# Kernel optimization log

Measured on AMD Instinct MI355X. Metric: run time of the kernel, lower is better.

## Reference

```python
import jax, jax.numpy as jnp
import numpy as np

B, C, N, H = 4, 256, 1024, 8
D = C            # per-head q/k dim (out_channels defaults to in_channels)
DV = C           # per-head value/output dim (y_out_channels defaults to out_channels)


def setup_inputs() -> dict:
    key = jax.random.key(0)
    ks = jax.random.split(key, 10)
    s = 0.02
    return {
        "x": jax.random.normal(ks[0], (B, C, N), jnp.float32),
        "y": jax.random.normal(ks[1], (B, C, N), jnp.float32),
        "Wq": jax.random.normal(ks[2], (H * D, C), jnp.float32) * s,
        "bq": jnp.zeros((H * D,), jnp.float32),
        "Wk": jax.random.normal(ks[3], (H * D, C), jnp.float32) * s,
        "bk": jnp.zeros((H * D,), jnp.float32),
        "Wv": jax.random.normal(ks[4], (H * DV, C), jnp.float32) * s,
        "bv": jnp.zeros((H * DV,), jnp.float32),
        "Wp": jax.random.normal(ks[5], (DV, C), jnp.float32) * s,  # projection, bias=False
        "gamma": jax.random.uniform(ks[6], (H, 1, 1, 1), jnp.float32) + 0.001,
    }


def _pconv(t, W, b):
    # 1x1 conv1d: (O,C) x (B,C,N) -> (B,O,N)
    out = jnp.einsum('oc,bcn->bon', W, t)
    return out if b is None else out + b[None, :, None]


def reference(x, y, Wq, bq, Wk, bk, Wv, bv, Wp, gamma):
    b_, _, n_ = x.shape
    h = gamma.shape[0]
    # Q/K/V projections, split channels into h heads (head-major chunks of D)
    q = _pconv(x, Wq, bq).reshape(b_, h, -1, n_)   # [B,H,D,N]
    k = _pconv(x, Wk, bk).reshape(b_, h, -1, n_)   # [B,H,D,N]
    v = _pconv(y, Wv, bv).reshape(b_, h, -1, n_)   # [B,H,DV,N]
    # energy[i,j] = sum_d q[d,i]*k[d,j]; softmax over keys j (no sqrt(d) scaling)
    attn = jax.nn.softmax(jnp.einsum('bhdn,bhdm->bhnm', q, k), axis=-1)
    out = jnp.einsum('bhdm,bhnm->bhdn', v, attn)   # [B,H,DV,N]
    # residual branch: y projected to DV channels (1x1 conv, no bias)
    yp = jnp.einsum('oc,bcn->bon', Wp, y)          # [B,DV,N]
    g = gamma.reshape(1, h, 1, 1)
    out = (g * out + yp[:, None, :, :]) / (1.0 + g)
    # concat heads along channel dim (head-major), matching split_cat(out,1,0,2)
    return out.reshape(b_, -1, n_)                 # [B,H*DV,N]
```

## Files before the change

kernel.cpp:

```cpp
#include <hip/hip_runtime.h>

#define Bb 4
#define Cc 256
#define Nn 1024
#define Hh 8
#define Oo 2048

typedef __attribute__((ext_vector_type(8))) short bf16x8;
typedef __attribute__((ext_vector_type(4))) float f32x4;

__device__ __forceinline__ short f2bf(float f) {
  unsigned u = __builtin_bit_cast(unsigned, f);
  unsigned r = u + 0x7FFFu + ((u >> 16) & 1u);
  return (short)(r >> 16);
}
__device__ __forceinline__ f32x4 mfma16(bf16x8 a, bf16x8 b, f32x4 c) {
  return __builtin_amdgcn_mfma_f32_16x16x32_bf16(a, b, c, 0, 0, 0);
}
__device__ __forceinline__ void gl_lds16(const void* g, void* l) {
  __builtin_amdgcn_global_load_lds(
      (const __attribute__((address_space(1))) void*)g,
      (__attribute__((address_space(3))) void*)l, 16, 0, 0);
}

__device__ __forceinline__ void stage_row512(const char* gbase, char* lds,
                                             int wave, int lane) {
#pragma unroll
  for (int i = 0; i < 8; i++) {
    int off = (wave * 8 + i) * 1024;
    int L = off + lane * 16;
    int r = L >> 9;
    int c = ((L >> 4) & 31) ^ (r & 7);
    gl_lds16(gbase + r * 512 + c * 16, lds + off);
  }
}
__device__ __forceinline__ void stage_row512_8(const char* gbase, char* lds,
                                               int wave, int lane) {
#pragma unroll
  for (int i = 0; i < 4; i++) {
    int off = (wave * 4 + i) * 1024;
    int L = off + lane * 16;
    int r = L >> 9;
    int c = ((L >> 4) & 31) ^ (r & 7);
    gl_lds16(gbase + r * 512 + c * 16, lds + off);
  }
}
__device__ __forceinline__ void stage_v8(const char* Vg, char* lds, int k0,
                                         int wave, int lane) {
#pragma unroll
  for (int i = 0; i < 4; i++) {
    int off = (wave * 4 + i) * 1024;
    int L = off + lane * 16;
    int r = L >> 7;
    int c = ((L >> 4) & 7) ^ (r & 7);
    gl_lds16(Vg + (size_t)r * 2048 + k0 * 2 + c * 16, lds + off);
  }
}

__global__ __launch_bounds__(256) void k_transpose(
    const float* __restrict__ x, const float* __restrict__ y,
    short* __restrict__ xT, short* __restrict__ yT,
    const float* __restrict__ Wq, const float* __restrict__ Wk,
    const float* __restrict__ Wv, const float* __restrict__ Wp,
    short* __restrict__ dWq, short* __restrict__ dWk, short* __restrict__ dWv,
    short* __restrict__ dWp) {
  {
    const int NW = Oo * Cc;
    int lin = blockIdx.x + 16 * (blockIdx.y + 4 * blockIdx.z);
    for (int i = (lin * 256 + threadIdx.x) * 4; i < 3 * NW + Cc * Cc;
         i += 512 * 256 * 4) {
      const float* src;
      short* dst;
      int off;
      if (i < NW) {
        src = Wq; dst = dWq; off = i;
      } else if (i < 2 * NW) {
        src = Wk; dst = dWk; off = i - NW;
      } else if (i < 3 * NW) {
        src = Wv; dst = dWv; off = i - 2 * NW;
      } else {
        src = Wp; dst = dWp; off = i - 3 * NW;
      }
      float4 v = *(const float4*)(src + off);
      short4 o;
      o.x = f2bf(v.x);
      o.y = f2bf(v.y);
      o.z = f2bf(v.z);
      o.w = f2bf(v.w);
      *(short4*)(dst + off) = o;
    }
  }
  int bz = blockIdx.z;
  int b = bz >> 1;
  const float* src = (bz & 1) ? y : x;
  short* dst = (bz & 1) ? yT : xT;
  src += (size_t)b * Cc * Nn;
  dst += (size_t)b * Nn * Cc;
  __shared__ short tile[64][68];
  int n0 = blockIdx.x * 64, c0 = blockIdx.y * 64;
  int t = threadIdx.x;
#pragma unroll
  for (int i = 0; i < 4; i++) {
    int idx = t + i * 256;
    int cc = idx >> 4, ng = idx & 15;
    float4 v = *(const float4*)(src + (size_t)(c0 + cc) * Nn + n0 + ng * 4);
    short4 o;
    o.x = f2bf(v.x);
    o.y = f2bf(v.y);
    o.z = f2bf(v.z);
    o.w = f2bf(v.w);
    *(short4*)&tile[cc][ng * 4] = o;
  }
  __syncthreads();
#pragma unroll
  for (int i = 0; i < 4; i++) {
    int idx = t + i * 256;
    int nn = idx >> 4, c4 = idx & 15;
    short4 o;
    o.x = tile[c4 * 4 + 0][nn];
    o.y = tile[c4 * 4 + 1][nn];
    o.z = tile[c4 * 4 + 2][nn];
    o.w = tile[c4 * 4 + 3][nn];
    *(short4*)(dst + (size_t)(n0 + nn) * Cc + c0 + c4 * 4) = o;
  }
}

__global__ __launch_bounds__(256, 4) void k_proj(
    const short* __restrict__ xT, const short* __restrict__ yT,
    const short* __restrict__ Wqb, const float* __restrict__ bq,
    const short* __restrict__ Wkb, const float* __restrict__ bk,
    const short* __restrict__ Wvb, const float* __restrict__ bv,
    const short* __restrict__ Wpb, short* __restrict__ Qt,
    short* __restrict__ Kt, short* __restrict__ Vv, float* __restrict__ yp) {
  int b = blockIdx.z, n0 = blockIdx.x * 64;
  int yb = blockIdx.y;
  int path = yb >> 5;
  int o0 = (yb & 31) * 64;
  const short* W = path == 0 ? Wqb : path == 1 ? Wkb : path == 2 ? Wvb : Wpb;
  bool dataStaged = path >= 2;
  int wave = threadIdx.x >> 6, lane = threadIdx.x & 63;
  int quad = lane >> 4, l16 = lane & 15;
  int sw = l16 & 7;
  __shared__ short Ws[64 * 256];

  const char* stage_src =
      dataStaged ? (const char*)(yT + (size_t)b * Nn * Cc + (size_t)n0 * Cc)
                 : (const char*)(W + (size_t)o0 * Cc);
  stage_row512(stage_src, (char*)Ws, wave, lane);

  const short* aptr =
      dataStaged
          ? W + (size_t)(o0 + wave * 16 + l16) * Cc + quad * 8
          : xT + (size_t)b * Nn * Cc + (size_t)(n0 + wave * 16 + l16) * Cc +
                quad * 8;
  bf16x8 areg[8];
#pragma unroll
  for (int ks = 0; ks < 8; ks++) areg[ks] = *(const bf16x8*)(aptr + ks * 32);

  f32x4 acc[4];
#pragma unroll
  for (int j = 0; j < 4; j++) acc[j] = f32x4{0.f, 0.f, 0.f, 0.f};
  __syncthreads();
#pragma unroll
  for (int ks = 0; ks < 8; ks++) {
#pragma unroll
    for (int cj = 0; cj < 4; cj++) {
      int off = (cj * 16 + l16) * 512 + (((ks * 4 + quad) ^ sw) << 4);
      bf16x8 wf = *(const bf16x8*)((const char*)Ws + off);
      if (dataStaged)
        acc[cj] = mfma16(areg[ks], wf, acc[cj]);
      else
        acc[cj] = mfma16(wf, areg[ks], acc[cj]);
    }
  }
  if (path < 2) {
    short* Od = path == 0 ? Qt : Kt;
    const float* bias = path == 0 ? bq : bk;
#pragma unroll
    for (int cj = 0; cj < 4; cj++) {
      int obase = o0 + cj * 16 + quad * 4;
      int h = obase >> 8, d = obase & 255;
      int n = n0 + wave * 16 + l16;
      float4 vb = *(const float4*)(bias + obase);
      size_t idx = (((size_t)(b * Hh + h) * Nn) + n) * 256 + d;
      short4 o;
      o.x = f2bf(acc[cj][0] + vb.x);
      o.y = f2bf(acc[cj][1] + vb.y);
      o.z = f2bf(acc[cj][2] + vb.z);
      o.w = f2bf(acc[cj][3] + vb.w);
      *(short4*)(Od + idx) = o;
    }
  } else {
#pragma unroll
    for (int cj = 0; cj < 4; cj++) {
      int n = n0 + cj * 16 + l16;
#pragma unroll
      for (int r = 0; r < 4; r++) {
        int o = o0 + wave * 16 + quad * 4 + r;
        if (path == 3) {
          yp[((size_t)b * Cc + o) * Nn + n] = acc[cj][r];
        } else {
          float v = acc[cj][r] + bv[o];
          Vv[((size_t)b * Oo + o) * Nn + n] = f2bf(v);
        }
      }
    }
  }
}

__global__ __launch_bounds__(512, 4) void k_attn(
    const short* __restrict__ Qt, const short* __restrict__ Kt,
    const short* __restrict__ Vv, const float* __restrict__ yp,
    const float* __restrict__ gamma, float* __restrict__ out) {
  int id = blockIdx.x;
  int bh = (id & 7) * 4 + (id >> 7);
  int q0 = ((id >> 3) & 15) * 64;
  int b = bh >> 3, h = bh & 7;
  int wave = threadIdx.x >> 6, lane = threadIdx.x & 63;
  int wq = wave >> 1, wk = wave & 1;
  int quad = lane >> 4, l16 = lane & 15;
  int sw = l16 & 7;
  const short* Qb = Qt + (size_t)bh * Nn * 256;
  const char* Kg = (const char*)(Kt + (size_t)bh * Nn * 256);
  const char* Vg = (const char*)(Vv + (size_t)bh * 256 * Nn);

  __shared__ short Klds[64 * 256];
  __shared__ short Vlds[256 * 64];
  __shared__ short plds[4][16][64];
  __shared__ float llds[2][64];

  bf16x8 qreg[8];
  {
    const short* qp = Qb + (size_t)(q0 + wq * 16 + l16) * 256 + quad * 8;
#pragma unroll
    for (int ks = 0; ks < 8; ks++) qreg[ks] = *(const bf16x8*)(qp + ks * 32);
  }
  f32x4 oacc[8];
#pragma unroll
  for (int j = 0; j < 8; j++) oacc[j] = f32x4{0.f, 0.f, 0.f, 0.f};
  float l_i[4] = {0.f, 0.f, 0.f, 0.f};

  stage_row512_8(Kg, (char*)Klds, wave, lane);
  stage_v8(Vg, (char*)Vlds, 0, wave, lane);

  for (int kt = 0; kt < 16; kt++) {
    int k0 = kt * 64;
    __syncthreads();
    f32x4 sc[2];
#pragma unroll
    for (int j = 0; j < 2; j++) sc[j] = f32x4{0.f, 0.f, 0.f, 0.f};
#pragma unroll
    for (int ks = 0; ks < 8; ks++) {
      bf16x8 kb0 = *(const bf16x8*)((const char*)Klds +
                                    (wk * 32 + l16) * 512 +
                                    (((ks * 4 + quad) ^ sw) << 4));
      bf16x8 kb1 = *(const bf16x8*)((const char*)Klds +
                                    (wk * 32 + 16 + l16) * 512 +
                                    (((ks * 4 + quad) ^ sw) << 4));
      sc[0] = mfma16(qreg[ks], kb0, sc[0]);
      sc[1] = mfma16(qreg[ks], kb1, sc[1]);
    }
#pragma unroll
    for (int cj = 0; cj < 2; cj++) {
#pragma unroll
      for (int r = 0; r < 4; r++) {
        float p = __expf(sc[cj][r]);
        l_i[r] += p;
        int row = quad * 4 + r;
        int keyhi = wk * 4 + cj * 2 + (l16 >> 3);
        plds[wq][row][((keyhi ^ (row & 7)) << 3) | sw] = f2bf(p);
      }
    }
    __syncthreads();
    if (kt < 15)
      stage_row512_8(Kg + (size_t)(k0 + 64) * 512, (char*)Klds, wave, lane);
#pragma unroll
    for (int c = 0; c < 2; c++) {
      bf16x8 ap[4];
#pragma unroll
      for (int qb = 0; qb < 4; qb++)
        ap[qb] = *(const bf16x8*)&plds[qb][l16][((c * 4 + quad) ^ sw) << 3];
#pragma unroll
      for (int dj = 0; dj < 2; dj++) {
        const char* vrow =
            (const char*)Vlds + (wave * 32 + dj * 16 + l16) * 128;
        bf16x8 v = *(const bf16x8*)(vrow + (((c * 4 + quad) ^ sw) << 4));
#pragma unroll
        for (int qb = 0; qb < 4; qb++)
          oacc[qb * 2 + dj] = mfma16(ap[qb], v, oacc[qb * 2 + dj]);
      }
    }
    __syncthreads();
    if (kt < 15) stage_v8(Vg, (char*)Vlds, k0 + 64, wave, lane);
  }
#pragma unroll
  for (int r = 0; r < 4; r++) {
    float v = l_i[r];
    v += __shfl_xor(v, 1);
    v += __shfl_xor(v, 2);
    v += __shfl_xor(v, 4);
    v += __shfl_xor(v, 8);
    l_i[r] = v;
  }
  if (l16 == 0) {
    f32x4 lv;
#pragma unroll
    for (int r = 0; r < 4; r++) lv[r] = l_i[r];
    *(f32x4*)&llds[wk][wq * 16 + quad * 4] = lv;
  }
  __syncthreads();
  float gf = gamma[h];
  float sg = gf / (1.f + gf), sy = 1.f / (1.f + gf);
#pragma unroll
  for (int qb = 0; qb < 4; qb++) {
    f32x4 lva = *(const f32x4*)&llds[0][qb * 16 + quad * 4];
    f32x4 lvb = *(const f32x4*)&llds[1][qb * 16 + quad * 4];
    int qq = q0 + qb * 16 + quad * 4;
#pragma unroll
    for (int dj = 0; dj < 2; dj++) {
      int dv = wave * 32 + dj * 16 + l16;
      const float* ypp = yp + ((size_t)b * 256 + dv) * Nn + qq;
      float* op = out + ((size_t)b * Oo + h * 256 + dv) * Nn + qq;
      float4 yv = *(const float4*)ypp;
      f32x4 oa = oacc[qb * 2 + dj];
      float4 ov;
      ov.x = sg * (oa[0] / (lva[0] + lvb[0])) + sy * yv.x;
      ov.y = sg * (oa[1] / (lva[1] + lvb[1])) + sy * yv.y;
      ov.z = sg * (oa[2] / (lva[2] + lvb[2])) + sy * yv.z;
      ov.w = sg * (oa[3] / (lva[3] + lvb[3])) + sy * yv.w;
      *(float4*)op = ov;
    }
  }
}

extern "C" void kernel_launch(void* const* d_in, const int* in_sizes, int n_in,
                              void* d_out, int out_size, void* d_ws,
                              size_t ws_size, hipStream_t stream) {
  const float* x = (const float*)d_in[0];
  const float* y = (const float*)d_in[1];
  const float* Wq = (const float*)d_in[2];
  const float* bq = (const float*)d_in[3];
  const float* Wk = (const float*)d_in[4];
  const float* bk = (const float*)d_in[5];
  const float* Wv = (const float*)d_in[6];
  const float* bv = (const float*)d_in[7];
  const float* Wp = (const float*)d_in[8];
  const float* gamma = (const float*)d_in[9];
  float* out = (float*)d_out;

  char* w = (char*)d_ws;
  short* Qt = (short*)(w + 0);
  short* Kt = (short*)(w + 16777216);
  short* Vv = (short*)(w + 33554432);
  short* xT = (short*)(w + 50331648);
  short* yT = (short*)(w + 52428800);
  float* yp = (float*)(w + 54525952);
  short* Wqb = (short*)(w + 58720256);
  short* Wkb = (short*)(w + 59768832);
  short* Wvb = (short*)(w + 60817408);
  short* Wpb = (short*)(w + 61865984);

  k_transpose<<<dim3(Nn / 64, Cc / 64, 2 * Bb), dim3(256), 0, stream>>>(
      x, y, xT, yT, Wq, Wk, Wv, Wp, Wqb, Wkb, Wvb, Wpb);
  k_proj<<<dim3(Nn / 64, 100, Bb), dim3(256), 0, stream>>>(
      xT, yT, Wqb, bq, Wkb, bk, Wvb, bv, Wpb, Qt, Kt, Vv, yp);
  k_attn<<<dim3(512), dim3(512), 0, stream>>>(Qt, Kt, Vv, yp, gamma, out);
}
```

Before: 192.2 us.

## Load V fragments straight from global into registers and restructure P/V work split

The attention kernel no longer stages V tiles through LDS. Each wave now loads its V fragments directly from global memory into registers, software-pipelined two deep across the head-dim blocks. The QK^T MFMA operands are swapped so P lands transposed and can be packed as bf16 pairs into a smaller LDS buffer. Each wave now owns a 16-query by 128-dim output tile instead of 64 by 32, which drops one barrier per key tile and the V LDS traffic. In exchange it adds uncoalesced, strided global reads of V that now sit on the critical path.

```diff
diff --git a/kernel.cpp b/kernel.cpp
--- a/kernel.cpp
+++ b/kernel.cpp
@@ -13,6 +13,10 @@
   unsigned u = __builtin_bit_cast(unsigned, f);
   unsigned r = u + 0x7FFFu + ((u >> 16) & 1u);
   return (short)(r >> 16);
+}
+__device__ __forceinline__ unsigned pk2(float a, float b) {
+  return ((unsigned)(unsigned short)f2bf(b) << 16) |
+         (unsigned)(unsigned short)f2bf(a);
 }
 __device__ __forceinline__ f32x4 mfma16(bf16x8 a, bf16x8 b, f32x4 c) {
   return __builtin_amdgcn_mfma_f32_16x16x32_bf16(a, b, c, 0, 0, 0);
@@ -43,17 +47,6 @@
     int r = L >> 9;
     int c = ((L >> 4) & 31) ^ (r & 7);
     gl_lds16(gbase + r * 512 + c * 16, lds + off);
-  }
-}
-__device__ __forceinline__ void stage_v8(const char* Vg, char* lds, int k0,
-                                         int wave, int lane) {
-#pragma unroll
-  for (int i = 0; i < 4; i++) {
-    int off = (wave * 4 + i) * 1024;
-    int L = off + lane * 16;
-    int r = L >> 7;
-    int c = ((L >> 4) & 7) ^ (r & 7);
-    gl_lds16(Vg + (size_t)r * 2048 + k0 * 2 + c * 16, lds + off);
   }
 }
 
@@ -225,8 +218,7 @@
   const char* Vg = (const char*)(Vv + (size_t)bh * 256 * Nn);
 
   __shared__ short Klds[64 * 256];
-  __shared__ short Vlds[256 * 64];
-  __shared__ short plds[4][16][64];
+  __shared__ unsigned plds32[4][16][36];
   __shared__ float llds[2][64];
 
   bf16x8 qreg[8];
@@ -238,17 +230,24 @@
   f32x4 oacc[8];
 #pragma unroll
   for (int j = 0; j < 8; j++) oacc[j] = f32x4{0.f, 0.f, 0.f, 0.f};
-  float l_i[4] = {0.f, 0.f, 0.f, 0.f};
+  float l_i = 0.f;
+
+  const char* vb0 = Vg + (size_t)(wk * 128 + l16) * 2048 + quad * 16;
 
   stage_row512_8(Kg, (char*)Klds, wave, lane);
-  stage_v8(Vg, (char*)Vlds, 0, wave, lane);
 
   for (int kt = 0; kt < 16; kt++) {
     int k0 = kt * 64;
     __syncthreads();
+    const char* vb = vb0 + (size_t)k0 * 2;
+    bf16x8 vf[2][2];
+    vf[0][0] = *(const bf16x8*)(vb);
+    vf[0][1] = *(const bf16x8*)(vb + 64);
+    vf[1][0] = *(const bf16x8*)(vb + 32768);
+    vf[1][1] = *(const bf16x8*)(vb + 32768 + 64);
     f32x4 sc[2];
-#pragma unroll
-    for (int j = 0; j < 2; j++) sc[j] = f32x4{0.f, 0.f, 0.f, 0.f};
+    sc[0] = f32x4{0.f, 0.f, 0.f, 0.f};
+    sc[1] = f32x4{0.f, 0.f, 0.f, 0.f};
 #pragma unroll
     for (int ks = 0; ks < 8; ks++) {
       bf16x8 kb0 = *(const bf16x8*)((const char*)Klds +
@@ -257,79 +256,65 @@
       bf16x8 kb1 = *(const bf16x8*)((const char*)Klds +
                                     (wk * 32 + 16 + l16) * 512 +
                                     (((ks * 4 + quad) ^ sw) << 4));
-      sc[0] = mfma16(qreg[ks], kb0, sc[0]);
-      sc[1] = mfma16(qreg[ks], kb1, sc[1]);
-    }
-#pragma unroll
-    for (int cj = 0; cj < 2; cj++) {
-#pragma unroll
-      for (int r = 0; r < 4; r++) {
-        float p = __expf(sc[cj][r]);
-        l_i[r] += p;
-        int row = quad * 4 + r;
-        int keyhi = wk * 4 + cj * 2 + (l16 >> 3);
-        plds[wq][row][((keyhi ^ (row & 7)) << 3) | sw] = f2bf(p);
-      }
-    }
+      sc[0] = mfma16(kb0, qreg[ks], sc[0]);
+      sc[1] = mfma16(kb1, qreg[ks], sc[1]);
+    }
+    float p0[4], p1[4];
+#pragma unroll
+    for (int r = 0; r < 4; r++) {
+      p0[r] = __expf(sc[0][r]);
+      p1[r] = __expf(sc[1][r]);
+      l_i += p0[r] + p1[r];
+    }
+    *(uint2*)&plds32[wq][l16][wk * 16 + 2 * quad] =
+        make_uint2(pk2(p0[0], p0[1]), pk2(p0[2], p0[3]));
+    *(uint2*)&plds32[wq][l16][wk * 16 + 8 + 2 * quad] =
+        make_uint2(pk2(p1[0], p1[1]), pk2(p1[2], p1[3]));
     __syncthreads();
     if (kt < 15)
       stage_row512_8(Kg + (size_t)(k0 + 64) * 512, (char*)Klds, wave, lane);
-#pragma unroll
-    for (int c = 0; c < 2; c++) {
-      bf16x8 ap[4];
-#pragma unroll
-      for (int qb = 0; qb < 4; qb++)
-        ap[qb] = *(const bf16x8*)&plds[qb][l16][((c * 4 + quad) ^ sw) << 3];
-#pragma unroll
-      for (int dj = 0; dj < 2; dj++) {
-        const char* vrow =
-            (const char*)Vlds + (wave * 32 + dj * 16 + l16) * 128;
-        bf16x8 v = *(const bf16x8*)(vrow + (((c * 4 + quad) ^ sw) << 4));
-#pragma unroll
-        for (int qb = 0; qb < 4; qb++)
-          oacc[qb * 2 + dj] = mfma16(ap[qb], v, oacc[qb * 2 + dj]);
+    bf16x8 pa0 = *(const bf16x8*)&plds32[wq][l16][4 * quad];
+    bf16x8 pa1 = *(const bf16x8*)&plds32[wq][l16][16 + 4 * quad];
+#pragma unroll
+    for (int dvb = 0; dvb < 8; dvb++) {
+      int cur = dvb & 1;
+      oacc[dvb] = mfma16(pa0, vf[cur][0], oacc[dvb]);
+      oacc[dvb] = mfma16(pa1, vf[cur][1], oacc[dvb]);
+      if (dvb < 6) {
+        const char* vn = vb + (size_t)(dvb + 2) * 32768;
+        vf[cur][0] = *(const bf16x8*)(vn);
+        vf[cur][1] = *(const bf16x8*)(vn + 64);
       }
     }
-    __syncthreads();
-    if (kt < 15) stage_v8(Vg, (char*)Vlds, k0 + 64, wave, lane);
-  }
-#pragma unroll
-  for (int r = 0; r < 4; r++) {
-    float v = l_i[r];
-    v += __shfl_xor(v, 1);
-    v += __shfl_xor(v, 2);
-    v += __shfl_xor(v, 4);
-    v += __shfl_xor(v, 8);
-    l_i[r] = v;
-  }
-  if (l16 == 0) {
-    f32x4 lv;
-#pragma unroll
-    for (int r = 0; r < 4; r++) lv[r] = l_i[r];
-    *(f32x4*)&llds[wk][wq * 16 + quad * 4] = lv;
+  }
+  {
+    float v = l_i;
+    v += __shfl_xor(v, 16);
+    v += __shfl_xor(v, 32);
+    if (lane < 16) llds[wk][wq * 16 + lane] = v;
   }
   __syncthreads();
   float gf = gamma[h];
   float sg = gf / (1.f + gf), sy = 1.f / (1.f + gf);
-#pragma unroll
-  for (int qb = 0; qb < 4; qb++) {
-    f32x4 lva = *(const f32x4*)&llds[0][qb * 16 + quad * 4];
-    f32x4 lvb = *(const f32x4*)&llds[1][qb * 16 + quad * 4];
-    int qq = q0 + qb * 16 + quad * 4;
-#pragma unroll
-    for (int dj = 0; dj < 2; dj++) {
-      int dv = wave * 32 + dj * 16 + l16;
-      const float* ypp = yp + ((size_t)b * 256 + dv) * Nn + qq;
-      float* op = out + ((size_t)b * Oo + h * 256 + dv) * Nn + qq;
-      float4 yv = *(const float4*)ypp;
-      f32x4 oa = oacc[qb * 2 + dj];
-      float4 ov;
-      ov.x = sg * (oa[0] / (lva[0] + lvb[0])) + sy * yv.x;
-      ov.y = sg * (oa[1] / (lva[1] + lvb[1])) + sy * yv.y;
-      ov.z = sg * (oa[2] / (lva[2] + lvb[2])) + sy * yv.z;
-      ov.w = sg * (oa[3] / (lva[3] + lvb[3])) + sy * yv.w;
-      *(float4*)op = ov;
-    }
+  f32x4 lva = *(const f32x4*)&llds[0][wq * 16 + quad * 4];
+  f32x4 lvb = *(const f32x4*)&llds[1][wq * 16 + quad * 4];
+  f32x4 linv;
+#pragma unroll
+  for (int r = 0; r < 4; r++) linv[r] = sg / (lva[r] + lvb[r]);
+  int qq = q0 + wq * 16 + quad * 4;
+#pragma unroll
+  for (int dvb = 0; dvb < 8; dvb++) {
+    int dv = wk * 128 + dvb * 16 + l16;
+    const float* ypp = yp + ((size_t)b * 256 + dv) * Nn + qq;
+    float* op = out + ((size_t)b * Oo + h * 256 + dv) * Nn + qq;
+    float4 yv = *(const float4*)ypp;
+    f32x4 oa = oacc[dvb];
+    float4 ov;
+    ov.x = linv[0] * oa[0] + sy * yv.x;
+    ov.y = linv[1] * oa[1] + sy * yv.y;
+    ov.z = linv[2] * oa[2] + sy * yv.z;
+    ov.w = linv[3] * oa[3] + sy * yv.w;
+    *(float4*)op = ov;
   }
 }
 
```

After: 266.7 us. 1.39x slower.
